# Performance work log

Measured on AMD Instinct MI355X. Metric: run time of the kernel, lower is better.

## Reference

```python
import jax, jax.numpy as jnp
import numpy as np

B, S, D, H = 2, 2048, 1024, 16
HD = D // H  # head_dim = 64


def setup_inputs() -> dict:
    key = jax.random.key(0)
    k1, k2, k3, k4, k5 = jax.random.split(key, 5)
    x = jax.random.normal(k1, (B, S, D), dtype=jnp.float32)
    # causal additive mask [S, S]: 0 on/below diagonal, -1e9 above
    mask = jnp.where(jnp.tril(jnp.ones((S, S), dtype=bool)), 0.0, -1e9).astype(jnp.float32)
    scale = 1.0 / np.sqrt(D)
    W_qkv = jax.random.normal(k2, (D, 3 * D), dtype=jnp.float32) * scale
    b_qkv = jax.random.normal(k3, (3 * D,), dtype=jnp.float32) * 0.01
    W_o = jax.random.normal(k4, (D, D), dtype=jnp.float32) * scale
    b_o = jax.random.normal(k5, (D,), dtype=jnp.float32) * 0.01
    return {"x": x, "mask": mask, "W_qkv": W_qkv, "b_qkv": b_qkv, "W_o": W_o, "b_o": b_o}


def reference(x, mask, W_qkv, b_qkv, W_o, b_o):
    b, s, d = x.shape
    qkv = x @ W_qkv + b_qkv                         # [B,S,3D]
    qkv = qkv.reshape(b, s, H, 3 * HD).transpose(0, 2, 1, 3)  # [B,H,S,3*HD]
    q, k, v = jnp.split(qkv, 3, axis=-1)            # each [B,H,S,HD]
    scores = jnp.einsum('bhqd,bhkd->bhqk', q, k) / np.sqrt(HD)  # [B,H,S,S]
    scores = scores + mask                           # broadcast [S,S] additive mask
    attn = jax.nn.softmax(scores, axis=-1)
    vals = jnp.einsum('bhqk,bhkd->bhqd', attn, v)    # [B,H,S,HD]
    vals = vals.transpose(0, 2, 1, 3).reshape(b, s, d)
    return vals @ W_o + b_o
```

## Files before the change

### kernel.cpp

```cpp
#include <hip/hip_runtime.h>

#define NB 2
#define NS 2048
#define ND 1024
#define NH 16
#define NHD 64
#define QLD (3 * ND)
#define PADP 72

typedef unsigned short u16;
typedef __attribute__((ext_vector_type(8))) short short8;
typedef __attribute__((ext_vector_type(4))) float f32x4;

__device__ __forceinline__ u16 f2b(float f) {
    unsigned int x = __float_as_uint(f);
    return (u16)((x + 0x7fffu + ((x >> 16) & 1u)) >> 16);
}

__device__ __forceinline__ unsigned int cvtpk(float lo, float hi) {
    unsigned int r;
    asm("v_cvt_pk_bf16_f32 %0, %1, %2" : "=v"(r) : "v"(lo), "v"(hi));
    return r;
}

__device__ __forceinline__ int swz8(int d) {
    return ((d >> 1) ^ (d >> 3)) & 7;
}

__global__ __launch_bounds__(256) void prep(
    const float* __restrict__ x, u16* __restrict__ x_bf,
    const float* __restrict__ Wqkv, u16* __restrict__ WqkvT,
    const float* __restrict__ Wo, u16* __restrict__ WoT)
{
    __shared__ u16 Ts[64 * 72];
    const int bid = blockIdx.x;
    const int t = threadIdx.x;

    if (bid < 2048) {
        const int i = (bid * 256 + t) * 8;
        float4 a = *(const float4*)(x + i);
        float4 b = *(const float4*)(x + i + 4);
        *(ushort4*)(x_bf + i)     = make_ushort4(f2b(a.x), f2b(a.y), f2b(a.z), f2b(a.w));
        *(ushort4*)(x_bf + i + 4) = make_ushort4(f2b(b.x), f2b(b.y), f2b(b.z), f2b(b.w));
        return;
    }

    const float* W; u16* WT; int N, bx, by;
    if (bid < 2048 + 768) {
        const int r = bid - 2048;
        W = Wqkv; WT = WqkvT; N = QLD; bx = r % 48; by = r / 48;
    } else {
        const int r = bid - 2816;
        W = Wo; WT = WoT; N = ND; bx = r & 15; by = r >> 4;
    }
    const int K = ND;
    const int k0 = by << 6, n0 = bx << 6;
    const int rr0 = t >> 4, c = (t & 15) << 2;
    #pragma unroll
    for (int rr = 0; rr < 64; rr += 16) {
        float4 v = *(const float4*)&W[(size_t)(k0 + rr0 + rr) * N + n0 + c];
        Ts[(c + 0) * 72 + rr0 + rr] = f2b(v.x);
        Ts[(c + 1) * 72 + rr0 + rr] = f2b(v.y);
        Ts[(c + 2) * 72 + rr0 + rr] = f2b(v.z);
        Ts[(c + 3) * 72 + rr0 + rr] = f2b(v.w);
    }
    __syncthreads();
    const int n = t >> 2, cc = (t & 3) << 4;
    uint4 a = *(const uint4*)&Ts[n * 72 + cc];
    uint4 b = *(const uint4*)&Ts[n * 72 + cc + 8];
    *(uint4*)&WT[(size_t)(n0 + n) * K + k0 + cc]     = a;
    *(uint4*)&WT[(size_t)(n0 + n) * K + k0 + cc + 8] = b;
}

template <int BM, int BN, bool STORE_BF16>
__global__ __launch_bounds__(256) void gemm_mfma(
    const u16* __restrict__ A, const u16* __restrict__ BT,
    const float* __restrict__ bias,
    void* __restrict__ C, int M, int N, int K)
{
    constexpr int AIS = BM / 64;
    constexpr int BIS = BN / 64;
    constexpr int MI  = BM / 32;
    constexpr int NJ  = BN / 32;
    __shared__ u16 As[2][BM * 32];
    __shared__ u16 Bs[2][BN * 32];

    const int tid = threadIdx.x;
    const int wave = tid >> 6, lane = tid & 63;
    const int col = lane & 15, quad = lane >> 4;
    const int wm = wave >> 1, wn = wave & 1;

    const int nwgx = gridDim.x;
    const int wg = blockIdx.y * nwgx + blockIdx.x;
    const int cpx = (nwgx * gridDim.y) >> 3;
    const int swz = (wg & 7) * cpx + (wg >> 3);
    const int row0 = (swz / nwgx) * BM, col0 = (swz % nwgx) * BN;

    f32x4 acc[MI][NJ] = {};

    const u16* asrc[AIS];
    u16* adst[2][AIS];
    #pragma unroll
    for (int is = 0; is < AIS; ++is) {
        const int J = is * 256 + wave * 64 + lane;
        const int m = J >> 2;
        const int q = (J & 3) ^ ((m >> 1) & 3);
        asrc[is] = A + (size_t)(row0 + m) * K + q * 8;
        adst[0][is] = &As[0][(size_t)(is * 256 + wave * 64) * 8];
        adst[1][is] = &As[1][(size_t)(is * 256 + wave * 64) * 8];
    }
    const u16* bsrc[BIS];
    u16* bdst[2][BIS];
    #pragma unroll
    for (int is = 0; is < BIS; ++is) {
        const int J = is * 256 + wave * 64 + lane;
        const int m = J >> 2;
        const int q = (J & 3) ^ ((m >> 1) & 3);
        bsrc[is] = BT + (size_t)(col0 + m) * K + q * 8;
        bdst[0][is] = &Bs[0][(size_t)(is * 256 + wave * 64) * 8];
        bdst[1][is] = &Bs[1][(size_t)(is * 256 + wave * 64) * 8];
    }

    auto stage = [&](int buf, int kk) {
        #pragma unroll
        for (int is = 0; is < AIS; ++is)
            __builtin_amdgcn_global_load_lds(
                (const __attribute__((address_space(1))) unsigned int*)(asrc[is] + kk),
                (__attribute__((address_space(3))) unsigned int*)adst[buf][is], 16, 0, 0);
        #pragma unroll
        for (int is = 0; is < BIS; ++is)
            __builtin_amdgcn_global_load_lds(
                (const __attribute__((address_space(1))) unsigned int*)(bsrc[is] + kk),
                (__attribute__((address_space(3))) unsigned int*)bdst[buf][is], 16, 0, 0);
    };

    const int NT = K / 32;
    stage(0, 0);
    __syncthreads();

    for (int t = 0; t < NT; ++t) {
        const int cur = t & 1;
        if (t + 1 < NT) stage(cur ^ 1, (t + 1) * 32);

        short8 af[MI], bf[NJ];
        #pragma unroll
        for (int i = 0; i < MI; ++i) {
            const int m = wm * (BM / 2) + i * 16 + col;
            af[i] = *(const short8*)&As[cur][(m * 4 + (quad ^ ((m >> 1) & 3))) * 8];
        }
        #pragma unroll
        for (int j = 0; j < NJ; ++j) {
            const int n = wn * (BN / 2) + j * 16 + col;
            bf[j] = *(const short8*)&Bs[cur][(n * 4 + (quad ^ ((n >> 1) & 3))) * 8];
        }
        #pragma unroll
        for (int i = 0; i < MI; ++i)
            #pragma unroll
            for (int j = 0; j < NJ; ++j)
                acc[i][j] = __builtin_amdgcn_mfma_f32_16x16x32_bf16(
                    af[i], bf[j], acc[i][j], 0, 0, 0);

        if (t + 1 < NT) __syncthreads();
    }

    #pragma unroll
    for (int j = 0; j < NJ; ++j) {
        const int gc = col0 + wn * (BN / 2) + j * 16 + col;
        const float qs = (STORE_BF16 && (((gc >> 6) % 3) == 0)) ? 0.125f : 1.0f;
        const float bj = bias[gc];
        #pragma unroll
        for (int i = 0; i < MI; ++i) {
            const int gr = row0 + wm * (BM / 2) + i * 16 + quad * 4;
            #pragma unroll
            for (int r = 0; r < 4; ++r) {
                const float v = (acc[i][j][r] + bj) * qs;
                if (STORE_BF16)
                    ((u16*)C)[(size_t)(gr + r) * N + gc] = f2b(v);
                else
                    ((float*)C)[(size_t)(gr + r) * N + gc] = v;
            }
        }
    }
}

__global__ __launch_bounds__(256) void attn_kernel(
    const u16* __restrict__ qkv, u16* __restrict__ vals)
{
    __shared__ u16 Ks[2][64 * 64];
    __shared__ u16 Vt[2][64 * 64];
    __shared__ u16 Ps[64 * PADP];

    const int tid = threadIdx.x;
    const int wave = tid >> 6, lane = tid & 63;
    const int col = lane & 15, quad = lane >> 4;
    const int qtA = blockIdx.x;
    const int qtB = 31 - qtA;
    const int bh = blockIdx.y;
    const int b = bh >> 4, h = bh & 15;
    const size_t base = (size_t)b * NS * QLD + (size_t)h * (3 * NHD);
    const int qloc = wave * 16 + col;

    int Jrow[2], Jcol[2];
    #pragma unroll
    for (int is = 0; is < 2; ++is) {
        const int J = is * 256 + wave * 64 + lane;
        Jrow[is] = J >> 3;
        Jcol[is] = ((J & 7) ^ (Jrow[is] & 7)) << 3;
    }

    auto stage_tile = [&](int buf, int srow, int coloff) {
        #pragma unroll
        for (int is = 0; is < 2; ++is) {
            __builtin_amdgcn_global_load_lds(
                (const __attribute__((address_space(1))) unsigned int*)
                    (qkv + base + (size_t)(srow + Jrow[is]) * QLD + coloff + Jcol[is]),
                (__attribute__((address_space(3))) unsigned int*)
                    &Ks[buf][(size_t)(is * 256 + wave * 64) * 8], 16, 0, 0);
        }
    };
    auto read_frag = [&](int buf, int row, int half) -> short8 {
        const int blk = row * 8 + ((quad + (half << 2)) ^ (row & 7));
        return *(const short8*)&Ks[buf][blk << 3];
    };

    const int vtx = tid & 15, vty = tid >> 4;
    const int vk0 = vty << 2, vd0 = vtx << 2;
    auto load_vregs = [&](int kt, ushort4* vr) {
        const u16* vsrc = qkv + base + (size_t)(kt * 64 + vk0) * QLD + 2 * NHD + vd0;
        vr[0] = *(const ushort4*)(vsrc);
        vr[1] = *(const ushort4*)(vsrc + QLD);
        vr[2] = *(const ushort4*)(vsrc + 2 * QLD);
        vr[3] = *(const ushort4*)(vsrc + 3 * QLD);
    };
    const int vC = vty >> 1, vS = (vty & 1) << 2;
    auto write_vt = [&](int buf, const ushort4* vr) {
        #pragma unroll
        for (int i = 0; i < 4; ++i) {
            const int d = vd0 + i;
            u16* p = &Vt[buf][d * 64 + ((vC ^ swz8(d)) << 3) + vS];
            *(ushort4*)p = make_ushort4(((const u16*)&vr[0])[i],
                                        ((const u16*)&vr[1])[i],
                                        ((const u16*)&vr[2])[i],
                                        ((const u16*)&vr[3])[i]);
        }
    };

    stage_tile(0, qtA * 64, 0);
    stage_tile(1, qtB * 64, 0);
    __syncthreads();
    short8 bqA0 = read_frag(0, qloc, 0), bqA1 = read_frag(0, qloc, 1);
    short8 bqB0 = read_frag(1, qloc, 0), bqB1 = read_frag(1, qloc, 1);
    __syncthreads();

    f32x4 accA[4] = {}, accB[4] = {};
    float mA = -1e30f, lA = 0.f, mB = -1e30f, lB = 0.f;

    auto qk = [&](const short8& b0, const short8& b1,
                  short8 (&kb)[4][2], f32x4 (&s)[4]) {
        __builtin_amdgcn_s_setprio(1);
        #pragma unroll
        for (int kg = 0; kg < 4; ++kg) {
            s[kg] = __builtin_amdgcn_mfma_f32_16x16x32_bf16(kb[kg][0], b0, s[kg], 0, 0, 0);
            s[kg] = __builtin_amdgcn_mfma_f32_16x16x32_bf16(kb[kg][1], b1, s[kg], 0, 0, 0);
        }
        __builtin_amdgcn_s_setprio(0);
    };

    auto sm = [&](f32x4 (&s)[4], f32x4 (&acc)[4], float& m, float& lsum, bool diag) {
        if (diag) {
            #pragma unroll
            for (int kg = 0; kg < 4; ++kg)
                #pragma unroll
                for (int r = 0; r < 4; ++r)
                    if (kg * 16 + quad * 4 + r > qloc) s[kg][r] = -1e30f;
        }
        float mx = -1e30f;
        #pragma unroll
        for (int kg = 0; kg < 4; ++kg)
            mx = fmaxf(mx, fmaxf(fmaxf(s[kg][0], s[kg][1]), fmaxf(s[kg][2], s[kg][3])));
        mx = fmaxf(mx, __shfl_xor(mx, 16, 64));
        mx = fmaxf(mx, __shfl_xor(mx, 32, 64));
        if (!__all(mx <= m + 8.f)) {
            const float mn = fmaxf(m, mx);
            const float alpha = __expf(m - mn);
            m = mn;
            lsum *= alpha;
            #pragma unroll
            for (int dg = 0; dg < 4; ++dg)
                #pragma unroll
                for (int r = 0; r < 4; ++r) acc[dg][r] *= alpha;
        }
        float psum = 0.f;
        #pragma unroll
        for (int kg = 0; kg < 4; ++kg) {
            float p0 = __expf(s[kg][0] - m);
            float p1 = __expf(s[kg][1] - m);
            float p2 = __expf(s[kg][2] - m);
            float p3 = __expf(s[kg][3] - m);
            psum += (p0 + p1) + (p2 + p3);
            uint2 w;
            w.x = cvtpk(p0, p1);
            w.y = cvtpk(p2, p3);
            *(uint2*)&Ps[qloc * PADP + kg * 16 + quad * 4] = w;
        }
        lsum += psum;
    };

    auto pv = [&](short8 (&vb)[4][2], f32x4 (&acc)[4]) {
        short8 pb0 = *(const short8*)&Ps[qloc * PADP + quad * 8];
        short8 pb1 = *(const short8*)&Ps[qloc * PADP + 32 + quad * 8];
        __builtin_amdgcn_s_setprio(1);
        #pragma unroll
        for (int dg = 0; dg < 4; ++dg) {
            acc[dg] = __builtin_amdgcn_mfma_f32_16x16x32_bf16(vb[dg][0], pb0, acc[dg], 0, 0, 0);
            acc[dg] = __builtin_amdgcn_mfma_f32_16x16x32_bf16(vb[dg][1], pb1, acc[dg], 0, 0, 0);
        }
        __builtin_amdgcn_s_setprio(0);
    };

    ushort4 vr[4];
    stage_tile(0, 0, NHD);
    load_vregs(0, vr);
    write_vt(0, vr);

    for (int kt = 0; kt <= qtB; ++kt) {
        const int cur = kt & 1, nxt = cur ^ 1;
        __syncthreads();
        if (kt < qtB) {
            stage_tile(nxt, (kt + 1) * 64, NHD);
            load_vregs(kt + 1, vr);
        }

        short8 kb[4][2], vb[4][2];
        #pragma unroll
        for (int kg = 0; kg < 4; ++kg) {
            kb[kg][0] = read_frag(cur, kg * 16 + col, 0);
            kb[kg][1] = read_frag(cur, kg * 16 + col, 1);
        }
        #pragma unroll
        for (int dg = 0; dg < 4; ++dg) {
            const int n = dg * 16 + col;
            #pragma unroll
            for (int c = 0; c < 2; ++c)
                vb[dg][c] = *(const short8*)
                    &Vt[cur][n * 64 + (((4 * c + quad) ^ swz8(n)) << 3)];
        }

        {
            f32x4 s[4] = {};
            qk(bqB0, bqB1, kb, s);
            sm(s, accB, mB, lB, kt == qtB);
            pv(vb, accB);
        }
        if (kt <= qtA) {
            f32x4 s[4] = {};
            qk(bqA0, bqA1, kb, s);
            sm(s, accA, mA, lA, kt == qtA);
            pv(vb, accA);
        }

        if (kt < qtB) write_vt(nxt, vr);
    }

    {
        float l1 = lA + __shfl_xor(lA, 16, 64);
        const float inv = 1.f / (l1 + __shfl_xor(l1, 32, 64));
        const size_t rowoff = ((size_t)b * NS + qtA * 64 + qloc) * ND + h * NHD;
        #pragma unroll
        for (int dg = 0; dg < 4; ++dg) {
            uint2 o;
            o.x = cvtpk(accA[dg][0] * inv, accA[dg][1] * inv);
            o.y = cvtpk(accA[dg][2] * inv, accA[dg][3] * inv);
            *(uint2*)(vals + rowoff + dg * 16 + quad * 4) = o;
        }
    }
    {
        float l1 = lB + __shfl_xor(lB, 16, 64);
        const float inv = 1.f / (l1 + __shfl_xor(l1, 32, 64));
        const size_t rowoff = ((size_t)b * NS + qtB * 64 + qloc) * ND + h * NHD;
        #pragma unroll
        for (int dg = 0; dg < 4; ++dg) {
            uint2 o;
            o.x = cvtpk(accB[dg][0] * inv, accB[dg][1] * inv);
            o.y = cvtpk(accB[dg][2] * inv, accB[dg][3] * inv);
            *(uint2*)(vals + rowoff + dg * 16 + quad * 4) = o;
        }
    }
}

extern "C" void kernel_launch(void* const* d_in, const int* in_sizes, int n_in,
                              void* d_out, int out_size, void* d_ws, size_t ws_size,
                              hipStream_t stream)
{
    const float* x    = (const float*)d_in[0];
    const float* Wqkv = (const float*)d_in[2];
    const float* bqkv = (const float*)d_in[3];
    const float* Wo   = (const float*)d_in[4];
    const float* bo   = (const float*)d_in[5];
    float* out = (float*)d_out;

    u16* x_bf   = (u16*)d_ws;
    u16* WqkvT  = x_bf   + (size_t)4096 * 1024;
    u16* WoT    = WqkvT  + (size_t)3072 * 1024;
    u16* qkv    = WoT    + (size_t)1024 * 1024;
    u16* vals   = qkv    + (size_t)4096 * 3072;

    const int M = NB * NS;

    prep<<<dim3(2048 + 768 + 256), dim3(256), 0, stream>>>(
        x, x_bf, Wqkv, WqkvT, Wo, WoT);

    gemm_mfma<128, 128, true><<<dim3(QLD / 128, M / 128), dim3(256), 0, stream>>>(
        x_bf, WqkvT, bqkv, qkv, M, QLD, ND);
    attn_kernel<<<dim3(16, NB * NH), dim3(256), 0, stream>>>(qkv, vals);
    gemm_mfma<64, 64, false><<<dim3(ND / 64, M / 64), dim3(256), 0, stream>>>(
        vals, WoT, bo, out, M, ND, ND);
}
```

Measured before the change: 199.8 us.

## Split paired causal attention work across two blocks with split-KV combine

Doubles the attention grid. Each pair of query tiles (qtA, qtB) is now split across two blocks of about 16-17 KV phases each, and the long qtB row is split by KV range between them. Each block writes its partial output plus its running max and sum to workspace, and a new combine kernel merges the two partials for qtB. The Ps LDS buffer drops its padding and uses an XOR swizzle instead. This raises parallelism from 512 to 1024 blocks and shortens the per-block critical path. The cost is an extra kernel launch and fp32 partial traffic through global memory.

Measured after the change: 211.3 us. +5.8%, slower.

```diff
diff --git a/kernel.cpp b/kernel.cpp
--- a/kernel.cpp
+++ b/kernel.cpp
@@ -6,7 +6,6 @@
 #define NH 16
 #define NHD 64
 #define QLD (3 * ND)
-#define PADP 72
 
 typedef unsigned short u16;
 typedef __attribute__((ext_vector_type(8))) short short8;
@@ -184,21 +183,31 @@
 }
 
 __global__ __launch_bounds__(256) void attn_kernel(
-    const u16* __restrict__ qkv, u16* __restrict__ vals)
+    const u16* __restrict__ qkv, u16* __restrict__ vals,
+    float* __restrict__ O0, float* __restrict__ O1,
+    float2* __restrict__ ml0, float2* __restrict__ ml1)
 {
     __shared__ u16 Ks[2][64 * 64];
     __shared__ u16 Vt[2][64 * 64];
-    __shared__ u16 Ps[64 * PADP];
+    __shared__ u16 Ps[64 * 64];
 
     const int tid = threadIdx.x;
     const int wave = tid >> 6, lane = tid & 63;
     const int col = lane & 15, quad = lane >> 4;
-    const int qtA = blockIdx.x;
-    const int qtB = 31 - qtA;
+    const int role = blockIdx.x >> 4;
+    const int p = blockIdx.x & 15;
+    const int qtA = p, qtB = 31 - p;
+    const int nB = 15 - p;
+    const int NPH = (role == 0) ? 17 : 16;
     const int bh = blockIdx.y;
     const int b = bh >> 4, h = bh & 15;
     const size_t base = (size_t)b * NS * QLD + (size_t)h * (3 * NHD);
     const int qloc = wave * 16 + col;
+    const int psx = (col & 7) << 1;
+
+    auto kv_of = [&](int ph) {
+        return (role == 0) ? ph : (ph < nB ? 17 + ph : ph - nB);
+    };
 
     int Jrow[2], Jcol[2];
     #pragma unroll
@@ -237,19 +246,19 @@
         #pragma unroll
         for (int i = 0; i < 4; ++i) {
             const int d = vd0 + i;
-            u16* p = &Vt[buf][d * 64 + ((vC ^ swz8(d)) << 3) + vS];
-            *(ushort4*)p = make_ushort4(((const u16*)&vr[0])[i],
-                                        ((const u16*)&vr[1])[i],
-                                        ((const u16*)&vr[2])[i],
-                                        ((const u16*)&vr[3])[i]);
-        }
-    };
-
-    stage_tile(0, qtA * 64, 0);
-    stage_tile(1, qtB * 64, 0);
+            u16* pp = &Vt[buf][d * 64 + ((vC ^ swz8(d)) << 3) + vS];
+            *(ushort4*)pp = make_ushort4(((const u16*)&vr[0])[i],
+                                         ((const u16*)&vr[1])[i],
+                                         ((const u16*)&vr[2])[i],
+                                         ((const u16*)&vr[3])[i]);
+        }
+    };
+
+    stage_tile(0, qtB * 64, 0);
+    stage_tile(1, qtA * 64, 0);
     __syncthreads();
-    short8 bqA0 = read_frag(0, qloc, 0), bqA1 = read_frag(0, qloc, 1);
-    short8 bqB0 = read_frag(1, qloc, 0), bqB1 = read_frag(1, qloc, 1);
+    short8 bqB0 = read_frag(0, qloc, 0), bqB1 = read_frag(0, qloc, 1);
+    short8 bqA0 = read_frag(1, qloc, 0), bqA1 = read_frag(1, qloc, 1);
     __syncthreads();
 
     f32x4 accA[4] = {}, accB[4] = {};
@@ -301,14 +310,14 @@
             uint2 w;
             w.x = cvtpk(p0, p1);
             w.y = cvtpk(p2, p3);
-            *(uint2*)&Ps[qloc * PADP + kg * 16 + quad * 4] = w;
+            *(uint2*)&Ps[qloc * 64 + (((4 * kg + quad) ^ psx) << 2)] = w;
         }
         lsum += psum;
     };
 
     auto pv = [&](short8 (&vb)[4][2], f32x4 (&acc)[4]) {
-        short8 pb0 = *(const short8*)&Ps[qloc * PADP + quad * 8];
-        short8 pb1 = *(const short8*)&Ps[qloc * PADP + 32 + quad * 8];
+        short8 pb0 = *(const short8*)&Ps[qloc * 64 + (((2 * quad) ^ psx) << 2)];
+        short8 pb1 = *(const short8*)&Ps[qloc * 64 + (((2 * quad + 8) ^ psx) << 2)];
         __builtin_amdgcn_s_setprio(1);
         #pragma unroll
         for (int dg = 0; dg < 4; ++dg) {
@@ -319,16 +328,17 @@
     };
 
     ushort4 vr[4];
-    stage_tile(0, 0, NHD);
-    load_vregs(0, vr);
+    stage_tile(0, kv_of(0) * 64, NHD);
+    load_vregs(kv_of(0), vr);
     write_vt(0, vr);
 
-    for (int kt = 0; kt <= qtB; ++kt) {
-        const int cur = kt & 1, nxt = cur ^ 1;
+    for (int ph = 0; ph < NPH; ++ph) {
+        const int cur = ph & 1, nxt = cur ^ 1;
         __syncthreads();
-        if (kt < qtB) {
-            stage_tile(nxt, (kt + 1) * 64, NHD);
-            load_vregs(kt + 1, vr);
+        if (ph + 1 < NPH) {
+            const int nkv = kv_of(ph + 1);
+            stage_tile(nxt, nkv * 64, NHD);
+            load_vregs(nkv, vr);
         }
 
         short8 kb[4][2], vb[4][2];
@@ -346,25 +356,40 @@
                     &Vt[cur][n * 64 + (((4 * c + quad) ^ swz8(n)) << 3)];
         }
 
-        {
+        const int kv = kv_of(ph);
+        const bool isB = (role == 0) || (ph < nB);
+        if (isB) {
             f32x4 s[4] = {};
             qk(bqB0, bqB1, kb, s);
-            sm(s, accB, mB, lB, kt == qtB);
+            sm(s, accB, mB, lB, kv == qtB);
             pv(vb, accB);
-        }
-        if (kt <= qtA) {
+        } else {
             f32x4 s[4] = {};
             qk(bqA0, bqA1, kb, s);
-            sm(s, accA, mA, lA, kt == qtA);
+            sm(s, accA, mA, lA, kv == qtA);
             pv(vb, accA);
         }
 
-        if (kt < qtB) write_vt(nxt, vr);
-    }
+        if (ph + 1 < NPH) write_vt(nxt, vr);
+    }
+
+    auto reduce_l = [&](float l) {
+        float t = l + __shfl_xor(l, 16, 64);
+        return t + __shfl_xor(t, 32, 64);
+    };
+    const size_t u = (size_t)(p * 32 + bh);
 
     {
-        float l1 = lA + __shfl_xor(lA, 16, 64);
-        const float inv = 1.f / (l1 + __shfl_xor(l1, 32, 64));
+        const float lf = reduce_l(lB);
+        float* Op = (role == 0 ? O0 : O1) + u * 4096;
+        #pragma unroll
+        for (int dg = 0; dg < 4; ++dg)
+            *(f32x4*)&Op[qloc * 64 + dg * 16 + quad * 4] = accB[dg];
+        if (quad == 0)
+            (role == 0 ? ml0 : ml1)[u * 64 + qloc] = make_float2(mB, lf);
+    }
+    if (role == 1) {
+        const float inv = 1.f / reduce_l(lA);
         const size_t rowoff = ((size_t)b * NS + qtA * 64 + qloc) * ND + h * NHD;
         #pragma unroll
         for (int dg = 0; dg < 4; ++dg) {
@@ -374,17 +399,35 @@
             *(uint2*)(vals + rowoff + dg * 16 + quad * 4) = o;
         }
     }
-    {
-        float l1 = lB + __shfl_xor(lB, 16, 64);
-        const float inv = 1.f / (l1 + __shfl_xor(l1, 32, 64));
-        const size_t rowoff = ((size_t)b * NS + qtB * 64 + qloc) * ND + h * NHD;
-        #pragma unroll
-        for (int dg = 0; dg < 4; ++dg) {
-            uint2 o;
-            o.x = cvtpk(accB[dg][0] * inv, accB[dg][1] * inv);
-            o.y = cvtpk(accB[dg][2] * inv, accB[dg][3] * inv);
-            *(uint2*)(vals + rowoff + dg * 16 + quad * 4) = o;
-        }
+}
+
+__global__ __launch_bounds__(64) void combine(
+    const float* __restrict__ O0, const float* __restrict__ O1,
+    const float2* __restrict__ ml0, const float2* __restrict__ ml1,
+    u16* __restrict__ vals)
+{
+    const int u = blockIdx.x;
+    const int p = u >> 5, bh = u & 31;
+    const int qtB = 31 - p;
+    const int b = bh >> 4, h = bh & 15;
+    const int q = threadIdx.x;
+    const float2 a = ml0[(size_t)u * 64 + q];
+    const float2 c = ml1[(size_t)u * 64 + q];
+    const float ms = fmaxf(a.x, c.x);
+    const float w0 = __expf(a.x - ms), w1 = __expf(c.x - ms);
+    const float inv = 1.f / (w0 * a.y + w1 * c.y);
+    const float s0 = w0 * inv, s1 = w1 * inv;
+    const float* o0 = O0 + (size_t)u * 4096 + q * 64;
+    const float* o1 = O1 + (size_t)u * 4096 + q * 64;
+    u16* dst = vals + ((size_t)b * NS + qtB * 64 + q) * ND + h * NHD;
+    #pragma unroll
+    for (int dg = 0; dg < 16; ++dg) {
+        float4 x0 = *(const float4*)(o0 + dg * 4);
+        float4 x1 = *(const float4*)(o1 + dg * 4);
+        uint2 o;
+        o.x = cvtpk(s0 * x0.x + s1 * x1.x, s0 * x0.y + s1 * x1.y);
+        o.y = cvtpk(s0 * x0.z + s1 * x1.z, s0 * x0.w + s1 * x1.w);
+        *(uint2*)(dst + dg * 4) = o;
     }
 }
 
@@ -404,6 +447,10 @@
     u16* WoT    = WqkvT  + (size_t)3072 * 1024;
     u16* qkv    = WoT    + (size_t)1024 * 1024;
     u16* vals   = qkv    + (size_t)4096 * 3072;
+    float* O0   = (float*)(vals + (size_t)4096 * 1024);
+    float* O1   = O0 + (size_t)512 * 4096;
+    float2* ml0 = (float2*)(O1 + (size_t)512 * 4096);
+    float2* ml1 = ml0 + (size_t)512 * 64;
 
     const int M = NB * NS;
 
@@ -412,7 +459,9 @@
 
     gemm_mfma<128, 128, true><<<dim3(QLD / 128, M / 128), dim3(256), 0, stream>>>(
         x_bf, WqkvT, bqkv, qkv, M, QLD, ND);
-    attn_kernel<<<dim3(16, NB * NH), dim3(256), 0, stream>>>(qkv, vals);
+    attn_kernel<<<dim3(32, NB * NH), dim3(256), 0, stream>>>(
+        qkv, vals, O0, O1, ml0, ml1);
+    combine<<<dim3(512), dim3(64), 0, stream>>>(O0, O1, ml0, ml1, vals);
     gemm_mfma<64, 64, false><<<dim3(ND / 64, M / 64), dim3(256), 0, stream>>>(
         vals, WoT, bo, out, M, ND, ND);
 }
```
